# Kernel optimization log

Hardware: AMD Instinct MI355X
Metric: run time of the kernel (lower is better)

Reference implementation:

```python
import jax, jax.numpy as jnp
import numpy as np

N = 50000
IN_CH = 128
HID = 32
HEADS = 3
OUT_CH = 128
E = 800000
NEG_SLOPE = 0.2
BN_EPS = 1e-5


def _glorot(key, shape):
    fan = shape[0] + shape[-1]
    s = jnp.sqrt(6.0 / fan)
    return jax.random.uniform(key, shape, jnp.float32, -s, s)


def setup_inputs() -> dict:
    key = jax.random.key(0)
    ks = jax.random.split(key, 12)
    x = jax.random.normal(ks[0], (N, IN_CH), jnp.float32)
    edge_index = jax.random.randint(ks[1], (2, E), 0, N, jnp.int64)
    # GATConv 1: in -> HID per head, HEADS heads, concat
    W1 = _glorot(ks[2], (IN_CH, HEADS * HID))
    att_src1 = _glorot(ks[3], (HEADS, HID))
    att_dst1 = _glorot(ks[4], (HEADS, HID))
    b1 = jnp.zeros((HEADS * HID,), jnp.float32)
    # GATConv 2: HEADS*HID -> OUT_CH, 1 head
    W2 = _glorot(ks[5], (HEADS * HID, OUT_CH))
    att_src2 = _glorot(ks[6], (1, OUT_CH))
    att_dst2 = _glorot(ks[7], (1, OUT_CH))
    b2 = jnp.zeros((OUT_CH,), jnp.float32)
    # BatchNorm params
    bn_gamma = jnp.ones((OUT_CH,), jnp.float32)
    bn_beta = jnp.zeros((OUT_CH,), jnp.float32)
    # residual Linear
    Wres = _glorot(ks[8], (IN_CH, OUT_CH))
    bres = jnp.zeros((OUT_CH,), jnp.float32)
    return dict(x=x, edge_index=edge_index, W1=W1, att_src1=att_src1,
                att_dst1=att_dst1, b1=b1, W2=W2, att_src2=att_src2,
                att_dst2=att_dst2, b2=b2, bn_gamma=bn_gamma, bn_beta=bn_beta,
                Wres=Wres, bres=bres)


def gat_conv(x, W, a_src, a_dst, b, src, dst, n, heads, ch):
    """PyG GATConv (eval mode, self-loops already in src/dst)."""
    h = (x @ W).reshape(n, heads, ch)                    # [N,H,C]
    a_s = jnp.sum(h * a_src[None], axis=-1)              # [N,H]
    a_d = jnp.sum(h * a_dst[None], axis=-1)              # [N,H]
    e = a_s[src] + a_d[dst]                              # [E,H]
    e = jnp.where(e > 0, e, NEG_SLOPE * e)               # leaky_relu
    m = jax.ops.segment_max(e, dst, num_segments=n)      # softmax over edges into dst
    e = jnp.exp(e - m[dst])
    denom = jax.ops.segment_sum(e, dst, num_segments=n)
    alpha = e / (denom[dst] + 1e-16)                     # [E,H]
    out = jax.ops.segment_sum(h[src] * alpha[:, :, None], dst, num_segments=n)
    return out.reshape(n, heads * ch) + b


def reference(x, edge_index, W1, att_src1, att_dst1, b1, W2, att_src2,
              att_dst2, b2, bn_gamma, bn_beta, Wres, bres):
    n = x.shape[0]
    loop = jnp.arange(n, dtype=edge_index.dtype)
    src = jnp.concatenate([edge_index[0], loop])         # add self-loops (PyG default)
    dst = jnp.concatenate([edge_index[1], loop])
    residual = x @ Wres + bres
    out = gat_conv(x, W1, att_src1, att_dst1, b1, src, dst, n, HEADS, HID)
    out = gat_conv(out, W2, att_src2, att_dst2, b2, src, dst, n, 1, OUT_CH)
    # BatchNorm1d, training-mode batch statistics
    mu = jnp.mean(out, axis=0)
    var = jnp.var(out, axis=0)
    out = (out - mu) * jax.lax.rsqrt(var + BN_EPS) * bn_gamma + bn_beta
    out = jax.nn.relu(out)
    return out + residual
```

## Files before the change

### kernel.cpp

```cpp
#include <hip/hip_runtime.h>

#define NEG 0.2f
#define NEG_INF (-1e30f)

typedef __attribute__((ext_vector_type(8))) short bf16x8;
typedef __attribute__((ext_vector_type(4))) float f32x4;

__device__ __forceinline__ float leaky(float e) { return e > 0.f ? e : NEG * e; }

__device__ __forceinline__ unsigned short f2bf(float f) {
    unsigned int u = __float_as_uint(f);
    unsigned int r = u + 0x7fffu + ((u >> 16) & 1u);
    return (unsigned short)(r >> 16);
}
__device__ __forceinline__ float2 bf2f2(unsigned int u) {
    float2 r;
    r.x = __uint_as_float(u << 16);
    r.y = __uint_as_float(u & 0xffff0000u);
    return r;
}

__device__ __forceinline__ void pack_w(const float* __restrict__ W,
                                       unsigned short* __restrict__ Bp, int K, int N, int idx) {
    int i = idx & 7;
    int rest = idx >> 3;
    int lane = rest & 63;
    rest >>= 6;
    int KT = K / 32;
    int kt = rest % KT;
    int ct = rest / KT;
    int m = lane & 15, kb = lane >> 4;
    int k = kt * 32 + kb * 8 + i, col = ct * 16 + m;
    Bp[idx] = f2bf(W[(size_t)k * N + col]);
}

__global__ __launch_bounds__(256) void prep_kernel(const float* __restrict__ x,
                                                   unsigned short* __restrict__ xb, int n4,
                                                   const float* __restrict__ W1,
                                                   unsigned short* __restrict__ w1p,
                                                   const float* __restrict__ W2,
                                                   unsigned short* __restrict__ w2p,
                                                   const float* __restrict__ Wres,
                                                   unsigned short* __restrict__ wresp,
                                                   const int* __restrict__ dst, int E,
                                                   int* __restrict__ deg, int histBlks) {
    int b = blockIdx.x;
    if (b < histBlks) {
        for (int e = b * 256 + threadIdx.x; e < E; e += histBlks * 256)
            atomicAdd(&deg[dst[e]], 1);
        return;
    }
    b -= histBlks;
    int nxb = (n4 + 255) / 256;
    if (b < nxb) {
        int i = b * 256 + threadIdx.x;
        if (i < n4) {
            float4 v = ((const float4*)x)[i];
            ushort4 o;
            o.x = f2bf(v.x); o.y = f2bf(v.y); o.z = f2bf(v.z); o.w = f2bf(v.w);
            ((ushort4*)xb)[i] = o;
        }
        return;
    }
    b -= nxb;
    if (b < 48) { pack_w(W1, w1p, 128, 96, b * 256 + threadIdx.x); return; }
    b -= 48;
    if (b < 48) { pack_w(W2, w2p, 96, 128, b * 256 + threadIdx.x); return; }
    b -= 48;
    if (b < 64) { pack_w(Wres, wresp, 128, 128, b * 256 + threadIdx.x); }
}

__global__ void scan_part(const int* __restrict__ deg, int* __restrict__ offs,
                          int* __restrict__ bsum, int n) {
    __shared__ int buf[256];
    int i = blockIdx.x * 256 + threadIdx.x;
    int v = (i < n) ? deg[i] : 0;
    buf[threadIdx.x] = v;
    __syncthreads();
    for (int s = 1; s < 256; s <<= 1) {
        int t = (threadIdx.x >= s) ? buf[threadIdx.x - s] : 0;
        __syncthreads();
        buf[threadIdx.x] += t;
        __syncthreads();
    }
    if (i < n) offs[i + 1] = buf[threadIdx.x];
    if (threadIdx.x == 255) bsum[blockIdx.x] = buf[255];
}

__global__ void scan_bsum(int* __restrict__ bsum, int nb) {
    __shared__ int buf[256];
    int v = (threadIdx.x < nb) ? bsum[threadIdx.x] : 0;
    buf[threadIdx.x] = v;
    __syncthreads();
    for (int s = 1; s < 256; s <<= 1) {
        int t = (threadIdx.x >= s) ? buf[threadIdx.x - s] : 0;
        __syncthreads();
        buf[threadIdx.x] += t;
        __syncthreads();
    }
    if (threadIdx.x < nb) bsum[threadIdx.x] = buf[threadIdx.x] - v;
}

__global__ void scan_add(int* __restrict__ offs, const int* __restrict__ bsum, int n,
                         int* __restrict__ pairBase, int* __restrict__ bcur) {
    int i = blockIdx.x * 256 + threadIdx.x;
    if (i < n) {
        int v = offs[i + 1] + bsum[blockIdx.x];
        offs[i + 1] = v;
        if (((i + 1) & 31) == 0) {
            int b = (i + 1) >> 5;
            pairBase[b] = v;
            bcur[b] = v;
        }
    }
    if (i == 0) { offs[0] = 0; pairBase[0] = 0; bcur[0] = 0; }
}

__global__ __launch_bounds__(256) void bin_kernel(const int* __restrict__ src,
                                                  const int* __restrict__ dst, int E,
                                                  int* __restrict__ bcur,
                                                  int2* __restrict__ pairBuf, int nb) {
    __shared__ int2 stage[4096];
    __shared__ int hist[1600];
    __shared__ int base[1600];
    for (int c0 = blockIdx.x * 4096; c0 < E; c0 += gridDim.x * 4096) {
        int cnt = min(4096, E - c0);
        for (int b = threadIdx.x; b < nb; b += 256) hist[b] = 0;
        __syncthreads();
        for (int i = threadIdx.x; i < cnt; i += 256) {
            int s = src[c0 + i], d = dst[c0 + i];
            stage[i] = make_int2(s, d);
            atomicAdd(&hist[d >> 5], 1);
        }
        __syncthreads();
        for (int b = threadIdx.x; b < nb; b += 256) {
            int h = hist[b];
            if (h) base[b] = atomicAdd(&bcur[b], h);
            hist[b] = 0;
        }
        __syncthreads();
        for (int i = threadIdx.x; i < cnt; i += 256) {
            int2 p = stage[i];
            int b = p.y >> 5;
            int off = atomicAdd(&hist[b], 1);
            pairBuf[base[b] + off] = p;
        }
        __syncthreads();
    }
}

template <int K, int N, int HEADS>
__device__ __forceinline__ void gemm_body(int w, const unsigned short* __restrict__ A,
                                          const unsigned short* __restrict__ Bp,
                                          const float* __restrict__ bias,
                                          unsigned short* __restrict__ outB,
                                          const float* __restrict__ asrc,
                                          const float* __restrict__ adst,
                                          float* __restrict__ a_s,
                                          float* __restrict__ a_d, int M) {
    constexpr int KT = K / 32, CT = N / 16;
    int row0 = w * 16;
    if (row0 >= M) return;
    int lane = threadIdx.x & 63;
    int m = lane & 15, kb = lane >> 4;
    const unsigned short* arow = A + (size_t)(row0 + m) * K + kb * 8;

    f32x4 acc[CT];
#pragma unroll
    for (int ct = 0; ct < CT; ++ct) acc[ct] = (f32x4){0.f, 0.f, 0.f, 0.f};

#pragma unroll
    for (int kt = 0; kt < KT; ++kt) {
        bf16x8 a = *(const bf16x8*)(arow + kt * 32);
#pragma unroll
        for (int ct = 0; ct < CT; ++ct) {
            bf16x8 b = *(const bf16x8*)(Bp + ((size_t)(ct * KT + kt) * 64 + lane) * 8);
            acc[ct] = __builtin_amdgcn_mfma_f32_16x16x32_bf16(a, b, acc[ct], 0, 0, 0);
        }
    }

#pragma unroll
    for (int r = 0; r < 4; ++r) {
        int row = row0 + kb * 4 + r;
#pragma unroll
        for (int ct = 0; ct < CT; ++ct) {
            int col = ct * 16 + m;
            float v = acc[ct][r] + (bias ? bias[col] : 0.f);
            outB[(size_t)row * N + col] = f2bf(v);
        }
    }

    if (HEADS > 0) {
        float asv[CT], adv[CT];
#pragma unroll
        for (int ct = 0; ct < CT; ++ct) {
            int col = ct * 16 + m;
            asv[ct] = asrc[col];
            adv[ct] = adst[col];
        }
        constexpr int TPH = CT / (HEADS > 0 ? HEADS : 1);
#pragma unroll
        for (int r = 0; r < 4; ++r) {
            int row = row0 + kb * 4 + r;
#pragma unroll
            for (int h = 0; h < HEADS; ++h) {
                float s = 0.f, d = 0.f;
#pragma unroll
                for (int t = 0; t < TPH; ++t) {
                    int ct = h * TPH + t;
                    s += acc[ct][r] * asv[ct];
                    d += acc[ct][r] * adv[ct];
                }
#pragma unroll
                for (int off = 1; off <= 8; off <<= 1) {
                    s += __shfl_xor(s, off);
                    d += __shfl_xor(d, off);
                }
                if (m == 0) {
                    a_s[(size_t)row * HEADS + h] = s;
                    a_d[(size_t)row * HEADS + h] = d;
                }
            }
        }
    }
}

__global__ __launch_bounds__(256) void phase2_kernel(
    const int2* __restrict__ pairBuf, const int* __restrict__ pairBase,
    const int* __restrict__ bcur, const int* __restrict__ offs,
    int* __restrict__ csr, int nb,
    const unsigned short* __restrict__ xb,
    const unsigned short* __restrict__ w1p, unsigned short* __restrict__ h1b,
    const float* __restrict__ asrc1, const float* __restrict__ adst1,
    float* __restrict__ as1, float* __restrict__ ad1,
    const unsigned short* __restrict__ wresp, const float* __restrict__ bres,
    unsigned short* __restrict__ residb, int n, int passBlks, int g1Blks) {
    int b = blockIdx.x;
    int lane = threadIdx.x & 63;
    int wid = threadIdx.x >> 6;
    if (b < passBlks) {
        __shared__ int cnt[4][32];
        int bk = b * 4 + wid;
        if (bk < nb) {
            int node0 = bk * 32;
            if (lane < 32) cnt[wid][lane] = (node0 + lane < n) ? offs[node0 + lane] : 0;
            int lo = pairBase[bk], hi = bcur[bk];
            for (int i = lo + lane; i < hi; i += 64) {
                int2 p = pairBuf[i];
                int pos = atomicAdd(&cnt[wid][p.y & 31], 1);
                csr[pos] = p.x;
            }
        }
        return;
    }
    b -= passBlks;
    if (b < g1Blks) {
        gemm_body<128, 96, 3>(b * 4 + wid, xb, w1p, nullptr, h1b,
                              asrc1, adst1, as1, ad1, n);
        return;
    }
    b -= g1Blks;
    gemm_body<128, 128, 0>(b * 4 + wid, xb, wresp, bres, residb,
                           nullptr, nullptr, nullptr, nullptr, n);
}

__global__ __launch_bounds__(256) void gemm2_kernel(const unsigned short* __restrict__ A,
                                                    const unsigned short* __restrict__ Bp,
                                                    unsigned short* __restrict__ outB,
                                                    const float* __restrict__ asrc,
                                                    const float* __restrict__ adst,
                                                    float* __restrict__ a_s,
                                                    float* __restrict__ a_d, int M) {
    gemm_body<96, 128, 1>(blockIdx.x * 4 + (threadIdx.x >> 6), A, Bp, nullptr, outB,
                          asrc, adst, a_s, a_d, M);
}

__global__ __launch_bounds__(256) void gat1_agg(const unsigned short* __restrict__ h1b,
                                                const float* __restrict__ a_s,
                                                const float* __restrict__ a_d,
                                                const int* __restrict__ offs,
                                                const int* __restrict__ csr,
                                                const float* __restrict__ b1,
                                                unsigned short* __restrict__ out1b, int n) {
    __shared__ int ssrc[4][64];
    __shared__ float se[4][3][64];
    int wid = threadIdx.x >> 6;
    int node = blockIdx.x * 4 + wid;
    if (node >= n) return;
    int lane = threadIdx.x & 63;
    int head = lane >> 4; if (head > 2) head = 2;
    int beg = offs[node], end = offs[node + 1];
    int deg = end - beg;
    float ad0 = a_d[node * 3 + 0], ad1 = a_d[node * 3 + 1], ad2 = a_d[node * 3 + 2];
    float es0 = leaky(a_s[node * 3 + 0] + ad0);
    float es1 = leaky(a_s[node * 3 + 1] + ad1);
    float es2 = leaky(a_s[node * 3 + 2] + ad2);
    float2 hv0 = make_float2(0.f, 0.f);
    if (lane < 48) hv0 = bf2f2(*(const unsigned int*)&h1b[(size_t)node * 96 + 2 * lane]);

    float den;
    float2 acc;

    if (deg <= 64) {
        int s = 0;
        float l0 = NEG_INF, l1 = NEG_INF, l2 = NEG_INF;
        if (lane < deg) {
            s = csr[beg + lane];
            l0 = leaky(a_s[s * 3 + 0] + ad0);
            l1 = leaky(a_s[s * 3 + 1] + ad1);
            l2 = leaky(a_s[s * 3 + 2] + ad2);
        }
        float m0 = l0, m1 = l1, m2 = l2;
#pragma unroll
        for (int sh = 32; sh >= 1; sh >>= 1) {
            m0 = fmaxf(m0, __shfl_xor(m0, sh));
            m1 = fmaxf(m1, __shfl_xor(m1, sh));
            m2 = fmaxf(m2, __shfl_xor(m2, sh));
        }
        m0 = fmaxf(m0, es0); m1 = fmaxf(m1, es1); m2 = fmaxf(m2, es2);
        float e0 = 0.f, e1 = 0.f, e2 = 0.f;
        if (lane < deg) {
            e0 = __expf(l0 - m0); e1 = __expf(l1 - m1); e2 = __expf(l2 - m2);
        }
        ssrc[wid][lane] = s;
        se[wid][0][lane] = e0; se[wid][1][lane] = e1; se[wid][2][lane] = e2;
        float w0 = __expf(es0 - m0), w1 = __expf(es1 - m1), w2 = __expf(es2 - m2);
        den = (head == 0) ? w0 : ((head == 1) ? w1 : w2);
        float wSelf = (lane < 16) ? w0 : ((lane < 32) ? w1 : w2);
        acc.x = wSelf * hv0.x; acc.y = wSelf * hv0.y;

        int jj = 0;
        for (; jj + 7 < deg; jj += 8) {
            int sA[8]; float wA[8]; unsigned ph[8];
#pragma unroll
            for (int q = 0; q < 8; ++q) {
                sA[q] = ssrc[wid][jj + q];
                wA[q] = se[wid][head][jj + q];
            }
#pragma unroll
            for (int q = 0; q < 8; ++q)
                ph[q] = (lane < 48) ? *(const unsigned*)&h1b[(size_t)sA[q] * 96 + 2 * lane] : 0u;
            float dsum = 0.f;
#pragma unroll
            for (int q = 0; q < 8; ++q) {
                dsum += wA[q];
                if (lane < 48) {
                    float2 h = bf2f2(ph[q]);
                    acc.x += wA[q] * h.x; acc.y += wA[q] * h.y;
                }
            }
            den += dsum;
        }
        for (; jj + 3 < deg; jj += 4) {
            int sA[4]; float wA[4]; unsigned ph[4];
#pragma unroll
            for (int q = 0; q < 4; ++q) {
                sA[q] = ssrc[wid][jj + q];
                wA[q] = se[wid][head][jj + q];
            }
#pragma unroll
            for (int q = 0; q < 4; ++q)
                ph[q] = (lane < 48) ? *(const unsigned*)&h1b[(size_t)sA[q] * 96 + 2 * lane] : 0u;
            float dsum = 0.f;
#pragma unroll
            for (int q = 0; q < 4; ++q) {
                dsum += wA[q];
                if (lane < 48) {
                    float2 h = bf2f2(ph[q]);
                    acc.x += wA[q] * h.x; acc.y += wA[q] * h.y;
                }
            }
            den += dsum;
        }
        for (; jj < deg; ++jj) {
            int sA = ssrc[wid][jj];
            float wA = se[wid][head][jj];
            den += wA;
            if (lane < 48) {
                float2 ha = bf2f2(*(const unsigned*)&h1b[(size_t)sA * 96 + 2 * lane]);
                acc.x += wA * ha.x; acc.y += wA * ha.y;
            }
        }
    } else {
        float m0 = es0, m1 = es1, m2 = es2;
        for (int j = beg + lane; j < end; j += 64) {
            int s = csr[j];
            m0 = fmaxf(m0, leaky(a_s[s * 3 + 0] + ad0));
            m1 = fmaxf(m1, leaky(a_s[s * 3 + 1] + ad1));
            m2 = fmaxf(m2, leaky(a_s[s * 3 + 2] + ad2));
        }
#pragma unroll
        for (int sh = 32; sh >= 1; sh >>= 1) {
            m0 = fmaxf(m0, __shfl_xor(m0, sh));
            m1 = fmaxf(m1, __shfl_xor(m1, sh));
            m2 = fmaxf(m2, __shfl_xor(m2, sh));
        }
        float w0 = __expf(es0 - m0), w1 = __expf(es1 - m1), w2 = __expf(es2 - m2);
        den = (head == 0) ? w0 : ((head == 1) ? w1 : w2);
        float wSelf = (lane < 16) ? w0 : ((lane < 32) ? w1 : w2);
        acc.x = wSelf * hv0.x; acc.y = wSelf * hv0.y;
        for (int t0 = beg; t0 < end; t0 += 64) {
            int cnt = min(64, end - t0);
            int s = 0;
            float e0 = 0.f, e1 = 0.f, e2 = 0.f;
            if (lane < cnt) {
                s = csr[t0 + lane];
                e0 = __expf(leaky(a_s[s * 3 + 0] + ad0) - m0);
                e1 = __expf(leaky(a_s[s * 3 + 1] + ad1) - m1);
                e2 = __expf(leaky(a_s[s * 3 + 2] + ad2) - m2);
            }
            ssrc[wid][lane] = s;
            se[wid][0][lane] = e0; se[wid][1][lane] = e1; se[wid][2][lane] = e2;
            int jj = 0;
            for (; jj + 7 < cnt; jj += 8) {
                int sA[8]; float wA[8]; unsigned ph[8];
#pragma unroll
                for (int q = 0; q < 8; ++q) {
                    sA[q] = ssrc[wid][jj + q];
                    wA[q] = se[wid][head][jj + q];
                }
#pragma unroll
                for (int q = 0; q < 8; ++q)
                    ph[q] = (lane < 48) ? *(const unsigned*)&h1b[(size_t)sA[q] * 96 + 2 * lane] : 0u;
                float dsum = 0.f;
#pragma unroll
                for (int q = 0; q < 8; ++q) {
                    dsum += wA[q];
                    if (lane < 48) {
                        float2 h = bf2f2(ph[q]);
                        acc.x += wA[q] * h.x; acc.y += wA[q] * h.y;
                    }
                }
                den += dsum;
            }
            for (; jj < cnt; ++jj) {
                int sA = ssrc[wid][jj];
                float wA = se[wid][head][jj];
                den += wA;
                if (lane < 48) {
                    float2 ha = bf2f2(*(const unsigned*)&h1b[(size_t)sA * 96 + 2 * lane]);
                    acc.x += wA * ha.x; acc.y += wA * ha.y;
                }
            }
        }
    }

    if (lane < 48) {
        float inv = 1.f / (den + 1e-16f);
        ushort2 o;
        o.x = f2bf(acc.x * inv + b1[2 * lane]);
        o.y = f2bf(acc.y * inv + b1[2 * lane + 1]);
        *(ushort2*)&out1b[(size_t)node * 96 + 2 * lane] = o;
    }
}

__global__ __launch_bounds__(256) void gat2_agg(const unsigned short* __restrict__ h2b,
                                                const float* __restrict__ a_s,
                                                const float* __restrict__ a_d,
                                                const int* __restrict__ offs,
                                                const int* __restrict__ csr,
                                                const float* __restrict__ b2,
                                                unsigned short* __restrict__ out2b,
                                                float* __restrict__ part, int n) {
    __shared__ int ssrc[4][64];
    __shared__ float se[4][64];
    __shared__ float4 red[4][64];
    int wid = threadIdx.x >> 6;
    int node = blockIdx.x * 4 + wid;
    int lane = threadIdx.x & 63;
    float2 o = make_float2(0.f, 0.f);

    if (node < n) {
        int beg = offs[node], end = offs[node + 1];
        int deg = end - beg;
        float ad = a_d[node];
        float es = leaky(a_s[node] + ad);
        float2 hv0 = bf2f2(*(const unsigned int*)&h2b[(size_t)node * 128 + 2 * lane]);
        float den;
        float2 acc;

        if (deg <= 64) {
            int s = 0;
            float l = NEG_INF;
            if (lane < deg) {
                s = csr[beg + lane];
                l = leaky(a_s[s] + ad);
            }
            float m = l;
#pragma unroll
            for (int sh = 32; sh >= 1; sh >>= 1) m = fmaxf(m, __shfl_xor(m, sh));
            m = fmaxf(m, es);
            float e = (lane < deg) ? __expf(l - m) : 0.f;
            ssrc[wid][lane] = s;
            se[wid][lane] = e;
            float wSelf = __expf(es - m);
            den = wSelf;
            acc.x = wSelf * hv0.x; acc.y = wSelf * hv0.y;

            int jj = 0;
            for (; jj + 7 < deg; jj += 8) {
                int sA[8]; float wA[8]; unsigned ph[8];
#pragma unroll
                for (int q = 0; q < 8; ++q) {
                    sA[q] = ssrc[wid][jj + q];
                    wA[q] = se[wid][jj + q];
                }
#pragma unroll
                for (int q = 0; q < 8; ++q)
                    ph[q] = *(const unsigned*)&h2b[(size_t)sA[q] * 128 + 2 * lane];
                float dsum = 0.f;
#pragma unroll
                for (int q = 0; q < 8; ++q) {
                    dsum += wA[q];
                    float2 h = bf2f2(ph[q]);
                    acc.x += wA[q] * h.x; acc.y += wA[q] * h.y;
                }
                den += dsum;
            }
            for (; jj + 3 < deg; jj += 4) {
                int sA[4]; float wA[4]; unsigned ph[4];
#pragma unroll
                for (int q = 0; q < 4; ++q) {
                    sA[q] = ssrc[wid][jj + q];
                    wA[q] = se[wid][jj + q];
                }
#pragma unroll
                for (int q = 0; q < 4; ++q)
                    ph[q] = *(const unsigned*)&h2b[(size_t)sA[q] * 128 + 2 * lane];
                float dsum = 0.f;
#pragma unroll
                for (int q = 0; q < 4; ++q) {
                    dsum += wA[q];
                    float2 h = bf2f2(ph[q]);
                    acc.x += wA[q] * h.x; acc.y += wA[q] * h.y;
                }
                den += dsum;
            }
            for (; jj < deg; ++jj) {
                int sA = ssrc[wid][jj];
                float wA = se[wid][jj];
                den += wA;
                float2 ha = bf2f2(*(const unsigned*)&h2b[(size_t)sA * 128 + 2 * lane]);
                acc.x += wA * ha.x; acc.y += wA * ha.y;
            }
        } else {
            float m = es;
            for (int j = beg + lane; j < end; j += 64) {
                int s = csr[j];
                m = fmaxf(m, leaky(a_s[s] + ad));
            }
#pragma unroll
            for (int sh = 32; sh >= 1; sh >>= 1) m = fmaxf(m, __shfl_xor(m, sh));
            float wSelf = __expf(es - m);
            den = wSelf;
            acc.x = wSelf * hv0.x; acc.y = wSelf * hv0.y;
            for (int t0 = beg; t0 < end; t0 += 64) {
                int cnt = min(64, end - t0);
                int s = 0;
                float e = 0.f;
                if (lane < cnt) {
                    s = csr[t0 + lane];
                    e = __expf(leaky(a_s[s] + ad) - m);
                }
                ssrc[wid][lane] = s;
                se[wid][lane] = e;
                int jj = 0;
                for (; jj + 7 < cnt; jj += 8) {
                    int sA[8]; float wA[8]; unsigned ph[8];
#pragma unroll
                    for (int q = 0; q < 8; ++q) {
                        sA[q] = ssrc[wid][jj + q];
                        wA[q] = se[wid][jj + q];
                    }
#pragma unroll
                    for (int q = 0; q < 8; ++q)
                        ph[q] = *(const unsigned*)&h2b[(size_t)sA[q] * 128 + 2 * lane];
                    float dsum = 0.f;
#pragma unroll
                    for (int q = 0; q < 8; ++q) {
                        dsum += wA[q];
                        float2 h = bf2f2(ph[q]);
                        acc.x += wA[q] * h.x; acc.y += wA[q] * h.y;
                    }
                    den += dsum;
                }
                for (; jj < cnt; ++jj) {
                    int sA = ssrc[wid][jj];
                    float wA = se[wid][jj];
                    den += wA;
                    float2 ha = bf2f2(*(const unsigned*)&h2b[(size_t)sA * 128 + 2 * lane]);
                    acc.x += wA * ha.x; acc.y += wA * ha.y;
                }
            }
        }

        float inv = 1.f / (den + 1e-16f);
        o.x = acc.x * inv + b2[2 * lane];
        o.y = acc.y * inv + b2[2 * lane + 1];
        ushort2 ob;
        ob.x = f2bf(o.x); ob.y = f2bf(o.y);
        *(ushort2*)&out2b[(size_t)node * 128 + 2 * lane] = ob;
    }

    red[wid][lane] = make_float4(o.x, o.y, o.x * o.x, o.y * o.y);
    __syncthreads();
    if (wid == 0) {
        float4 a = red[0][lane], b = red[1][lane], c = red[2][lane], d = red[3][lane];
        float sx = a.x + b.x + c.x + d.x;
        float sy = a.y + b.y + c.y + d.y;
        float qx = a.z + b.z + c.z + d.z;
        float qy = a.w + b.w + c.w + d.w;
        float* p = part + (size_t)(blockIdx.x & 63) * 256;
        atomicAdd(&p[2 * lane + 0], sx);
        atomicAdd(&p[2 * lane + 1], sy);
        atomicAdd(&p[128 + 2 * lane + 0], qx);
        atomicAdd(&p[128 + 2 * lane + 1], qy);
    }
}

__global__ void bn_finalize(const float* __restrict__ part, const float* __restrict__ gamma,
                            const float* __restrict__ beta, float* __restrict__ ss, int n) {
    int c = threadIdx.x;
    float S = 0.f, Q = 0.f;
    for (int k = 0; k < 64; ++k) {
        S += part[(size_t)k * 256 + c];
        Q += part[(size_t)k * 256 + 128 + c];
    }
    float invN = 1.f / (float)n;
    float mu = S * invN;
    float var = Q * invN - mu * mu;
    float g = gamma[c] * rsqrtf(var + 1e-5f);
    ss[c] = g;
    ss[128 + c] = beta[c] - mu * g;
}

__global__ void final_kernel(const unsigned short* __restrict__ out2b,
                             const unsigned short* __restrict__ residb,
                             const float* __restrict__ ss, float* __restrict__ out, int n) {
    int i = blockIdx.x * blockDim.x + threadIdx.x;
    if (i >= n * 32) return;
    int c0 = (i & 31) * 4;
    uint2 v = ((const uint2*)out2b)[i];
    uint2 r = ((const uint2*)residb)[i];
    float2 v01 = bf2f2(v.x), v23 = bf2f2(v.y);
    float2 r01 = bf2f2(r.x), r23 = bf2f2(r.y);
    float4 o;
    o.x = fmaxf(v01.x * ss[c0 + 0] + ss[128 + c0 + 0], 0.f) + r01.x;
    o.y = fmaxf(v01.y * ss[c0 + 1] + ss[128 + c0 + 1], 0.f) + r01.y;
    o.z = fmaxf(v23.x * ss[c0 + 2] + ss[128 + c0 + 2], 0.f) + r23.x;
    o.w = fmaxf(v23.y * ss[c0 + 3] + ss[128 + c0 + 3], 0.f) + r23.y;
    ((float4*)out)[i] = o;
}

extern "C" void kernel_launch(void* const* d_in, const int* in_sizes, int n_in,
                              void* d_out, int out_size, void* d_ws, size_t ws_size,
                              hipStream_t stream) {
    const float* x     = (const float*)d_in[0];
    const int*   ei    = (const int*)d_in[1];
    const float* W1    = (const float*)d_in[2];
    const float* asrc1 = (const float*)d_in[3];
    const float* adst1 = (const float*)d_in[4];
    const float* b1    = (const float*)d_in[5];
    const float* W2    = (const float*)d_in[6];
    const float* asrc2 = (const float*)d_in[7];
    const float* adst2 = (const float*)d_in[8];
    const float* b2    = (const float*)d_in[9];
    const float* gamma = (const float*)d_in[10];
    const float* beta  = (const float*)d_in[11];
    const float* Wres  = (const float*)d_in[12];
    const float* bres  = (const float*)d_in[13];

    const int n = in_sizes[0] / 128;
    const int E = in_sizes[1] / 2;

    char* ws = (char*)d_ws;
    size_t off = 0;
    auto alloc = [&](size_t bytes) {
        void* p = ws + off;
        off = (off + bytes + 255) & ~(size_t)255;
        return p;
    };
    float* as1  = (float*)alloc((size_t)n * 3 * 4);
    float* ad1  = (float*)alloc((size_t)n * 3 * 4);
    float* as2  = (float*)alloc((size_t)n * 4);
    float* ad2  = (float*)alloc((size_t)n * 4);
    float* part = (float*)alloc(64 * 256 * 4);
    float* ss   = (float*)alloc(256 * 4);
    unsigned short* xb     = (unsigned short*)alloc((size_t)n * 128 * 2);
    unsigned short* h1b    = (unsigned short*)alloc((size_t)n * 96 * 2);
    unsigned short* h2b    = (unsigned short*)alloc((size_t)n * 128 * 2);
    unsigned short* out1b  = (unsigned short*)alloc((size_t)n * 96 * 2);
    unsigned short* out2b  = (unsigned short*)alloc((size_t)n * 128 * 2);
    unsigned short* residb = (unsigned short*)alloc((size_t)n * 128 * 2);
    unsigned short* w1p    = (unsigned short*)alloc(128 * 96 * 2);
    unsigned short* w2p    = (unsigned short*)alloc(96 * 128 * 2);
    unsigned short* wresp  = (unsigned short*)alloc(128 * 128 * 2);
    int* deg      = (int*)alloc((size_t)n * 4);
    int* offs     = (int*)alloc((size_t)(n + 1) * 4);
    int* bsum     = (int*)alloc(256 * 4);
    int* pairBase = (int*)alloc(1600 * 4);
    int* bcur     = (int*)alloc(1600 * 4);
    int2* pairBuf = (int2*)alloc((size_t)E * 8);
    int* csr      = (int*)alloc((size_t)E * 4);

    hipMemsetAsync(deg, 0, (size_t)n * 4, stream);
    hipMemsetAsync(part, 0, 64 * 256 * 4, stream);

    const int* srcIdx = ei;
    const int* dstIdx = ei + E;
    const int nb = (n + 255) / 256;
    const int NB = (n + 31) / 32;

    const int histBlks = 512;
    const int nxb = (n * 32 + 255) / 256;
    prep_kernel<<<histBlks + nxb + 160, 256, 0, stream>>>(x, xb, n * 32, W1, w1p, W2, w2p,
                                                          Wres, wresp, dstIdx, E, deg, histBlks);

    scan_part<<<nb, 256, 0, stream>>>(deg, offs, bsum, n);
    scan_bsum<<<1, 256, 0, stream>>>(bsum, nb);
    scan_add<<<nb, 256, 0, stream>>>(offs, bsum, n, pairBase, bcur);

    bin_kernel<<<(E + 4095) / 4096, 256, 0, stream>>>(srcIdx, dstIdx, E, bcur, pairBuf, NB);

    const int mt = (n + 15) / 16;
    const int gblk = (mt + 3) / 4;
    const int passBlks = 391;

    phase2_kernel<<<passBlks + 2 * gblk, 256, 0, stream>>>(
        pairBuf, pairBase, bcur, offs, csr, NB, xb, w1p, h1b, asrc1, adst1, as1, ad1,
        wresp, bres, residb, n, passBlks, gblk);

    gat1_agg<<<(n + 3) / 4, 256, 0, stream>>>(h1b, as1, ad1, offs, csr, b1, out1b, n);
    gemm2_kernel<<<gblk, 256, 0, stream>>>(out1b, w2p, h2b, asrc2, adst2, as2, ad2, n);
    gat2_agg<<<(n + 3) / 4, 256, 0, stream>>>(h2b, as2, ad2, offs, csr, b2, out2b, part, n);
    bn_finalize<<<1, 128, 0, stream>>>(part, gamma, beta, ss, n);
    final_kernel<<<(n * 32 + 255) / 256, 256, 0, stream>>>(out2b, residb, ss, (float*)d_out, n);
}
```

Measured before the change: 191.4 us.

## Replace per-node degree histogram and 3-kernel scan with bucket counts

Instead of atomically counting per-node in-degree in global memory and running a three-kernel prefix scan over all nodes, the prep kernel now builds per-32-node bucket histograms in shared memory and flushes them with one atomic per bucket. A single 1024-thread kernel scans the bucket counts, and the per-node CSR offsets are derived inside phase2 by counting each bucket's pairs and doing a wave-level shuffle scan. This removes two kernel launches and most of the global atomic traffic, at the cost of an extra pass over pairBuf in phase2 and a serial single-block scan.

```diff
diff --git a/kernel.cpp b/kernel.cpp
--- a/kernel.cpp
+++ b/kernel.cpp
@@ -43,14 +43,25 @@
                                                    const float* __restrict__ Wres,
                                                    unsigned short* __restrict__ wresp,
                                                    const int* __restrict__ dst, int E,
-                                                   int* __restrict__ deg, int histBlks) {
+                                                   int* __restrict__ bucketCnt, int nbk,
+                                                   int binBlks) {
     int b = blockIdx.x;
-    if (b < histBlks) {
-        for (int e = b * 256 + threadIdx.x; e < E; e += histBlks * 256)
-            atomicAdd(&deg[dst[e]], 1);
+    if (b < binBlks) {
+        __shared__ int hist[1600];
+        for (int k = threadIdx.x; k < nbk; k += 256) hist[k] = 0;
+        __syncthreads();
+        int c0 = b * 4096;
+        int cnt = min(4096, E - c0);
+        for (int i = threadIdx.x; i < cnt; i += 256)
+            atomicAdd(&hist[dst[c0 + i] >> 5], 1);
+        __syncthreads();
+        for (int k = threadIdx.x; k < nbk; k += 256) {
+            int h = hist[k];
+            if (h) atomicAdd(&bucketCnt[k], h);
+        }
         return;
     }
-    b -= histBlks;
+    b -= binBlks;
     int nxb = (n4 + 255) / 256;
     if (b < nxb) {
         int i = b * 256 + threadIdx.x;
@@ -70,50 +81,41 @@
     if (b < 64) { pack_w(Wres, wresp, 128, 128, b * 256 + threadIdx.x); }
 }
 
-__global__ void scan_part(const int* __restrict__ deg, int* __restrict__ offs,
-                          int* __restrict__ bsum, int n) {
-    __shared__ int buf[256];
-    int i = blockIdx.x * 256 + threadIdx.x;
-    int v = (i < n) ? deg[i] : 0;
-    buf[threadIdx.x] = v;
+__global__ __launch_bounds__(1024) void scan_buckets(const int* __restrict__ bc,
+                                                     int* __restrict__ pairBase,
+                                                     int* __restrict__ bcur,
+                                                     int* __restrict__ offs, int nbk, int n) {
+    __shared__ int buf[1024];
+    __shared__ int carry;
+    int tid = threadIdx.x;
+    if (tid == 0) carry = 0;
     __syncthreads();
-    for (int s = 1; s < 256; s <<= 1) {
-        int t = (threadIdx.x >= s) ? buf[threadIdx.x - s] : 0;
-        __syncthreads();
-        buf[threadIdx.x] += t;
-        __syncthreads();
-    }
-    if (i < n) offs[i + 1] = buf[threadIdx.x];
-    if (threadIdx.x == 255) bsum[blockIdx.x] = buf[255];
-}
-
-__global__ void scan_bsum(int* __restrict__ bsum, int nb) {
-    __shared__ int buf[256];
-    int v = (threadIdx.x < nb) ? bsum[threadIdx.x] : 0;
-    buf[threadIdx.x] = v;
-    __syncthreads();
-    for (int s = 1; s < 256; s <<= 1) {
-        int t = (threadIdx.x >= s) ? buf[threadIdx.x - s] : 0;
-        __syncthreads();
-        buf[threadIdx.x] += t;
-        __syncthreads();
-    }
-    if (threadIdx.x < nb) bsum[threadIdx.x] = buf[threadIdx.x] - v;
-}
-
-__global__ void scan_add(int* __restrict__ offs, const int* __restrict__ bsum, int n,
-                         int* __restrict__ pairBase, int* __restrict__ bcur) {
-    int i = blockIdx.x * 256 + threadIdx.x;
-    if (i < n) {
-        int v = offs[i + 1] + bsum[blockIdx.x];
-        offs[i + 1] = v;
-        if (((i + 1) & 31) == 0) {
-            int b = (i + 1) >> 5;
-            pairBase[b] = v;
-            bcur[b] = v;
-        }
-    }
-    if (i == 0) { offs[0] = 0; pairBase[0] = 0; bcur[0] = 0; }
+    for (int base = 0; base < nbk; base += 1024) {
+        int v = (base + tid < nbk) ? bc[base + tid] : 0;
+        buf[tid] = v;
+        __syncthreads();
+        for (int s = 1; s < 1024; s <<= 1) {
+            int t = (tid >= s) ? buf[tid - s] : 0;
+            __syncthreads();
+            buf[tid] += t;
+            __syncthreads();
+        }
+        int incl = buf[tid];
+        int tot = buf[1023];
+        int c = carry;
+        if (base + tid < nbk) {
+            int ex = c + incl - v;
+            pairBase[base + tid] = ex;
+            bcur[base + tid] = ex;
+        }
+        __syncthreads();
+        if (tid == 0) carry = c + tot;
+        __syncthreads();
+    }
+    if (tid == 0) {
+        pairBase[nbk] = carry;
+        offs[n] = carry;
+    }
 }
 
 __global__ __launch_bounds__(256) void bin_kernel(const int* __restrict__ src,
@@ -227,7 +229,7 @@
 
 __global__ __launch_bounds__(256) void phase2_kernel(
     const int2* __restrict__ pairBuf, const int* __restrict__ pairBase,
-    const int* __restrict__ bcur, const int* __restrict__ offs,
+    const int* __restrict__ bcur, int* __restrict__ offs,
     int* __restrict__ csr, int nb,
     const unsigned short* __restrict__ xb,
     const unsigned short* __restrict__ w1p, unsigned short* __restrict__ h1b,
@@ -243,8 +245,22 @@
         int bk = b * 4 + wid;
         if (bk < nb) {
             int node0 = bk * 32;
-            if (lane < 32) cnt[wid][lane] = (node0 + lane < n) ? offs[node0 + lane] : 0;
             int lo = pairBase[bk], hi = bcur[bk];
+            if (lane < 32) cnt[wid][lane] = 0;
+            for (int i = lo + lane; i < hi; i += 64)
+                atomicAdd(&cnt[wid][pairBuf[i].y & 31], 1);
+            int myc = (lane < 32) ? cnt[wid][lane] : 0;
+            int c = myc;
+#pragma unroll
+            for (int s = 1; s < 32; s <<= 1) {
+                int t = __shfl_up(c, s);
+                if (lane >= s && lane < 32) c += t;
+            }
+            int basePos = lo + c - myc;
+            if (lane < 32) {
+                if (node0 + lane < n) offs[node0 + lane] = basePos;
+                cnt[wid][lane] = basePos;
+            }
             for (int i = lo + lane; i < hi; i += 64) {
                 int2 p = pairBuf[i];
                 int pos = atomicAdd(&cnt[wid][p.y & 31], 1);
@@ -695,32 +711,29 @@
     unsigned short* w1p    = (unsigned short*)alloc(128 * 96 * 2);
     unsigned short* w2p    = (unsigned short*)alloc(96 * 128 * 2);
     unsigned short* wresp  = (unsigned short*)alloc(128 * 128 * 2);
-    int* deg      = (int*)alloc((size_t)n * 4);
-    int* offs     = (int*)alloc((size_t)(n + 1) * 4);
-    int* bsum     = (int*)alloc(256 * 4);
-    int* pairBase = (int*)alloc(1600 * 4);
-    int* bcur     = (int*)alloc(1600 * 4);
-    int2* pairBuf = (int2*)alloc((size_t)E * 8);
-    int* csr      = (int*)alloc((size_t)E * 4);
-
-    hipMemsetAsync(deg, 0, (size_t)n * 4, stream);
+    int* offs      = (int*)alloc((size_t)(n + 1) * 4);
+    int* bucketCnt = (int*)alloc(1600 * 4);
+    int* pairBase  = (int*)alloc(1601 * 4);
+    int* bcur      = (int*)alloc(1600 * 4);
+    int2* pairBuf  = (int2*)alloc((size_t)E * 8);
+    int* csr       = (int*)alloc((size_t)E * 4);
+
+    hipMemsetAsync(bucketCnt, 0, 1600 * 4, stream);
     hipMemsetAsync(part, 0, 64 * 256 * 4, stream);
 
     const int* srcIdx = ei;
     const int* dstIdx = ei + E;
-    const int nb = (n + 255) / 256;
     const int NB = (n + 31) / 32;
-
-    const int histBlks = 512;
+    const int binBlks = (E + 4095) / 4096;
+
     const int nxb = (n * 32 + 255) / 256;
-    prep_kernel<<<histBlks + nxb + 160, 256, 0, stream>>>(x, xb, n * 32, W1, w1p, W2, w2p,
-                                                          Wres, wresp, dstIdx, E, deg, histBlks);
-
-    scan_part<<<nb, 256, 0, stream>>>(deg, offs, bsum, n);
-    scan_bsum<<<1, 256, 0, stream>>>(bsum, nb);
-    scan_add<<<nb, 256, 0, stream>>>(offs, bsum, n, pairBase, bcur);
-
-    bin_kernel<<<(E + 4095) / 4096, 256, 0, stream>>>(srcIdx, dstIdx, E, bcur, pairBuf, NB);
+    prep_kernel<<<binBlks + nxb + 160, 256, 0, stream>>>(x, xb, n * 32, W1, w1p, W2, w2p,
+                                                         Wres, wresp, dstIdx, E,
+                                                         bucketCnt, NB, binBlks);
+
+    scan_buckets<<<1, 1024, 0, stream>>>(bucketCnt, pairBase, bcur, offs, NB, n);
+
+    bin_kernel<<<binBlks, 256, 0, stream>>>(srcIdx, dstIdx, E, bcur, pairBuf, NB);
 
     const int mt = (n + 15) / 16;
     const int gblk = (mt + 3) / 4;
```

Measured after the change: 164.9 us. 13.8% less time.
